# Performance work log

Measured on AMD Instinct MI355X. Metric: run time of the kernel, lower is better.

Reference implementation:

```python
import jax, jax.numpy as jnp
import numpy as np

N_HEADS = 12

def setup_inputs() -> dict:
    key = jax.random.key(0)
    k1, k2, k3 = jax.random.split(key, 3)
    B, S, W = 8, 1024, 768
    x = jax.random.normal(k1, (B, S, W), dtype=jnp.float32)
    w_qkv = jax.random.normal(k2, (W, 3 * W), dtype=jnp.float32) * (W ** -0.5)
    w_out = jax.random.normal(k3, (W, W), dtype=jnp.float32) * (W ** -0.5)
    return {"x": x, "w_qkv": w_qkv, "w_out": w_out}

def reference(x, w_qkv, w_out):
    B, S, W = x.shape
    H = N_HEADS
    D = W // H  # head_width
    scale = W ** -0.5  # NOTE: source scales by width**-0.5, not head_width**-0.5
    qkv = x @ w_qkv  # [B, S, 3W]
    q, k, v = jnp.split(qkv, 3, axis=2)
    q = q.reshape(B, S, H, D)
    k = k.reshape(B, S, H, D)
    # attn_score: [B, i, j, n]
    attn_score = jnp.einsum('binh,bjnh->bijn', q, k) * scale
    attn_weight = jax.nn.softmax(attn_score, axis=2)
    # NOTE: source uses K (not V) here — faithful reproduction of the bug.
    out = jnp.einsum('bijn,bjnh->binh', attn_weight, k)
    out = out.reshape(B, S, W)
    return out @ w_out  # dropout is identity in eval
```

## Files before the change

### kernel.cpp

```cpp
#include <hip/hip_runtime.h>

#define US unsigned short

typedef __bf16 bf16x8 __attribute__((ext_vector_type(8)));
typedef short s16x8 __attribute__((ext_vector_type(8)));
typedef short s16x4 __attribute__((ext_vector_type(4)));
typedef float f32x4 __attribute__((ext_vector_type(4)));

static __device__ __forceinline__ US f2bf(float f) {
  union { float f; unsigned u; } x; x.f = f;
  unsigned r = x.u + 0x7fffu + ((x.u >> 16) & 1u);
  return (US)(r >> 16);
}

static __device__ __forceinline__ unsigned cvtpk(float lo, float hi) {
  unsigned r;
  asm("v_cvt_pk_bf16_f32 %0, %1, %2" : "=v"(r) : "v"(lo), "v"(hi));
  return r;
}

static __device__ __forceinline__ void gload16(const US* g, US* l) {
  __builtin_amdgcn_global_load_lds(
      (const __attribute__((address_space(1))) void*)g,
      (__attribute__((address_space(3))) void*)l, 16, 0, 0);
}

__global__ __launch_bounds__(256) void cast_f32_bf16(
    const float* __restrict__ src, US* __restrict__ dst) {
  int i = blockIdx.x * 256 + threadIdx.x;
  const float4* s = (const float4*)src + (size_t)i * 2;
  float4 a = s[0], b = s[1];
  s16x8 w;
  w[0] = (short)f2bf(a.x); w[1] = (short)f2bf(a.y);
  w[2] = (short)f2bf(a.z); w[3] = (short)f2bf(a.w);
  w[4] = (short)f2bf(b.x); w[5] = (short)f2bf(b.y);
  w[6] = (short)f2bf(b.z); w[7] = (short)f2bf(b.w);
  *(s16x8*)(dst + (size_t)i * 8) = w;
}

__global__ __launch_bounds__(256) void transpose_cast_k(
    const float* __restrict__ src, US* __restrict__ dst, int R, int C,
    float scale, int nlim) {
  __shared__ float t[32][33];
  int n0 = blockIdx.x * 32, r0 = blockIdx.y * 32;
  int tx = threadIdx.x & 31, ty = threadIdx.x >> 5;
  for (int i = 0; i < 4; ++i) {
    int r = i * 8 + ty;
    t[r][tx] = src[(size_t)(r0 + r) * C + n0 + tx];
  }
  __syncthreads();
  for (int i = 0; i < 4; ++i) {
    int n = i * 8 + ty;
    float s = (n0 + n < nlim) ? scale : 1.0f;
    dst[(size_t)(n0 + n) * R + r0 + tx] = f2bf(t[tx][n] * s);
  }
}

__global__ __launch_bounds__(256) void kt_transpose(
    const US* __restrict__ QK, US* __restrict__ KT) {
  __shared__ US t[32][34];
  int bh = blockIdx.z, b = bh / 12, h = bh % 12;
  int s0 = blockIdx.x * 32, d0 = blockIdx.y * 32;
  int tx = threadIdx.x & 31, ty = threadIdx.x >> 5;
  const US* src = QK + ((size_t)b * 1024 + s0) * 1536 + 768 + h * 64 + d0;
  for (int i = 0; i < 4; ++i)
    t[i * 8 + ty][tx] = src[(size_t)(i * 8 + ty) * 1536 + tx];
  __syncthreads();
  US* dst = KT + ((size_t)bh * 64 + d0) * 1024 + s0;
  for (int i = 0; i < 4; ++i)
    dst[(size_t)(i * 8 + ty) * 1024 + tx] = t[tx][i * 8 + ty];
}

template<int OUT_BF16>
__global__ __launch_bounds__(256) void gemm_bt(
    const US* __restrict__ A, const US* __restrict__ Bt,
    void* __restrict__ Cv, int M, int N, int K) {
  __shared__ US As[2][128 * 32];
  __shared__ US Bs[2][128 * 32];
  const int tid = threadIdx.x;
  const int wave = tid >> 6, lane = tid & 63;
  const int lr = lane & 15, lg = lane >> 4;
  const int m0 = blockIdx.x * 128, n0 = blockIdx.y * 128;
  const int wr = (wave >> 1) * 64, wc = (wave & 1) * 64;
  const int srow = tid >> 2;
  const int sseg = (tid & 3) ^ (srow & 3);
  const US* gA = A + (size_t)(m0 + srow) * K + sseg * 8;
  const US* gB = Bt + (size_t)(n0 + srow) * K + sseg * 8;

  f32x4 acc[4][4];
  for (int i = 0; i < 4; ++i)
    for (int j = 0; j < 4; ++j) acc[i][j] = (f32x4){0.f, 0.f, 0.f, 0.f};

  const int nIt = K >> 5;
  for (int i = 0; i < 2; ++i) {
    gload16(gA + (size_t)i * 64 * K, &As[0][tid * 8 + i * 2048]);
    gload16(gB + (size_t)i * 64 * K, &Bs[0][tid * 8 + i * 2048]);
  }
  __syncthreads();

  for (int it = 0; it < nIt; ++it) {
    if (it + 1 < nIt) {
      int k0 = (it + 1) * 32, bb = (it + 1) & 1;
      for (int i = 0; i < 2; ++i) {
        gload16(gA + (size_t)i * 64 * K + k0, &As[bb][tid * 8 + i * 2048]);
        gload16(gB + (size_t)i * 64 * K + k0, &Bs[bb][tid * 8 + i * 2048]);
      }
    }
    const US* Ab = As[it & 1];
    const US* Bb = Bs[it & 1];
    bf16x8 af[4], bfr[4];
    for (int mi = 0; mi < 4; ++mi)
      af[mi] = *(const bf16x8*)(Ab + (wr + mi * 16 + lr) * 32 + ((lg ^ (lr & 3)) * 8));
    for (int ni = 0; ni < 4; ++ni)
      bfr[ni] = *(const bf16x8*)(Bb + (wc + ni * 16 + lr) * 32 + ((lg ^ (lr & 3)) * 8));
    for (int mi = 0; mi < 4; ++mi)
      for (int ni = 0; ni < 4; ++ni)
        acc[mi][ni] = __builtin_amdgcn_mfma_f32_16x16x32_bf16(
            af[mi], bfr[ni], acc[mi][ni], 0, 0, 0);
    __syncthreads();
  }

  for (int mi = 0; mi < 4; ++mi)
    for (int ni = 0; ni < 4; ++ni)
      for (int r = 0; r < 4; ++r) {
        size_t row = (size_t)m0 + wr + mi * 16 + lg * 4 + r;
        size_t col = (size_t)n0 + wc + ni * 16 + lr;
        float v = acc[mi][ni][r];
        if (OUT_BF16) ((US*)Cv)[row * N + col] = f2bf(v);
        else          ((float*)Cv)[row * N + col] = v;
      }
}

static __device__ __forceinline__ void softmax_route(
    const f32x4 sv[4], float& lsum, bool odd, bool hi, int laneQ0, int laneQ1,
    bf16x8& pa0v, bf16x8& pa1v) {
  float p[4][4];
#pragma unroll
  for (int ns = 0; ns < 4; ++ns)
#pragma unroll
    for (int r = 0; r < 4; ++r) {
      p[ns][r] = __builtin_amdgcn_exp2f(sv[ns][r]);
      lsum += p[ns][r];
    }
  unsigned pk00 = cvtpk(p[0][0], p[0][1]), pk01 = cvtpk(p[0][2], p[0][3]);
  unsigned pk10 = cvtpk(p[1][0], p[1][1]), pk11 = cvtpk(p[1][2], p[1][3]);
  unsigned pk20 = cvtpk(p[2][0], p[2][1]), pk21 = cvtpk(p[2][2], p[2][3]);
  unsigned pk30 = cvtpk(p[3][0], p[3][1]), pk31 = cvtpk(p[3][2], p[3][3]);
  int a0 = (int)(odd ? pk10 : pk00), a1 = (int)(odd ? pk11 : pk01);
  int a2 = (int)(odd ? pk30 : pk20), a3 = (int)(odd ? pk31 : pk21);
  int b0 = (int)(odd ? pk00 : pk10), b1 = (int)(odd ? pk01 : pk11);
  int b2 = (int)(odd ? pk20 : pk30), b3 = (int)(odd ? pk21 : pk31);
  int r0 = __shfl(a0, laneQ0), r1 = __shfl(a1, laneQ0);
  int r2 = __shfl(a2, laneQ0), r3 = __shfl(a3, laneQ0);
  int r4 = __shfl(b0, laneQ1), r5 = __shfl(b1, laneQ1);
  int r6 = __shfl(b2, laneQ1), r7 = __shfl(b3, laneQ1);
  union { unsigned u[4]; bf16x8 v; } pa0, pa1;
  pa0.u[0] = hi ? (unsigned)r4 : (unsigned)r0;
  pa0.u[1] = hi ? (unsigned)r5 : (unsigned)r1;
  pa0.u[2] = hi ? (unsigned)r0 : (unsigned)r4;
  pa0.u[3] = hi ? (unsigned)r1 : (unsigned)r5;
  pa1.u[0] = hi ? (unsigned)r6 : (unsigned)r2;
  pa1.u[1] = hi ? (unsigned)r7 : (unsigned)r3;
  pa1.u[2] = hi ? (unsigned)r2 : (unsigned)r6;
  pa1.u[3] = hi ? (unsigned)r3 : (unsigned)r7;
  pa0v = pa0.v;
  pa1v = pa1.v;
}

__global__ __launch_bounds__(256, 3) void attn_kernel(
    const US* __restrict__ QK, const US* __restrict__ KTg, US* __restrict__ AO) {
  __shared__ US Kr[2][64 * 64];
  __shared__ US Kt[2][64 * 64];
  const int tid = threadIdx.x, wave = tid >> 6, lane = tid & 63;
  const int lr = lane & 15, lg = lane >> 4;
  const int id = blockIdx.y * 8 + blockIdx.x;
  const int bh = (id & 7) * 12 + ((id >> 3) % 12);
  const int qt = id / 96;
  const int b = bh / 12, h = bh % 12;
  const int qw = qt * 128 + wave * 32;
  const size_t rowbase = (size_t)b * 1024;
  const US* Qp = QK + rowbase * 1536 + h * 64;
  const US* Kp = QK + rowbase * 1536 + 768 + h * 64;
  const US* KTp = KTg + (size_t)bh * 64 * 1024;

  const int srow = tid >> 3;
  const int sseg = (tid & 7) ^ (srow & 7);
  const US* gK = Kp + (size_t)srow * 1536 + sseg * 8;
  const US* gT = KTp + (size_t)srow * 1024 + sseg * 8;

  bf16x8 qf0[2], qf1[2];
#pragma unroll
  for (int kk = 0; kk < 2; ++kk) {
    qf0[kk] = *(const bf16x8*)(Qp + (size_t)(qw + lr) * 1536 + kk * 32 + lg * 8);
    qf1[kk] = *(const bf16x8*)(Qp + (size_t)(qw + 16 + lr) * 1536 + kk * 32 + lg * 8);
  }

  const bool odd = (lg & 1) != 0;
  const bool hi = (lg >> 1) != 0;
  const int laneQ0 = lr + 32 * (lg & 1) + 16 * (lg >> 1);
  const int laneQ1 = lr + 32 * (lg & 1) + 16 * (1 - (lg >> 1));

  float lsum0 = 0.f, lsum1 = 0.f;
  f32x4 acc0[4], acc1[4];
#pragma unroll
  for (int d = 0; d < 4; ++d) {
    acc0[d] = (f32x4){0.f, 0.f, 0.f, 0.f};
    acc1[d] = (f32x4){0.f, 0.f, 0.f, 0.f};
  }

  for (int i = 0; i < 2; ++i) {
    gload16(gK + (size_t)(i * 32) * 1536, &Kr[0][tid * 8 + i * 2048]);
    gload16(gT + (size_t)(i * 32) * 1024, &Kt[0][tid * 8 + i * 2048]);
  }
  __syncthreads();

  for (int t = 0; t < 16; ++t) {
    if (t + 1 < 16) {
      int kv0 = (t + 1) * 64, bb = (t + 1) & 1;
      for (int i = 0; i < 2; ++i) {
        gload16(gK + (size_t)(kv0 + i * 32) * 1536, &Kr[bb][tid * 8 + i * 2048]);
        gload16(gT + (size_t)(i * 32) * 1024 + kv0, &Kt[bb][tid * 8 + i * 2048]);
      }
    }
    const US* Krb = Kr[t & 1];
    const US* Ktb = Kt[t & 1];

    f32x4 sv0[4], sv1[4];
    __builtin_amdgcn_s_setprio(1);
#pragma unroll
    for (int ns = 0; ns < 4; ++ns) {
      f32x4 a0 = {0.f, 0.f, 0.f, 0.f}, a1 = {0.f, 0.f, 0.f, 0.f};
#pragma unroll
      for (int kk = 0; kk < 2; ++kk) {
        bf16x8 kf = *(const bf16x8*)(
            Krb + (ns * 16 + lr) * 64 + (((kk * 4 + lg) ^ (lr & 7)) * 8));
        a0 = __builtin_amdgcn_mfma_f32_16x16x32_bf16(kf, qf0[kk], a0, 0, 0, 0);
        a1 = __builtin_amdgcn_mfma_f32_16x16x32_bf16(kf, qf1[kk], a1, 0, 0, 0);
      }
      sv0[ns] = a0; sv1[ns] = a1;
    }
    __builtin_amdgcn_s_setprio(0);

    bf16x8 pa00, pa01, pa10, pa11;
    softmax_route(sv0, lsum0, odd, hi, laneQ0, laneQ1, pa00, pa01);
    softmax_route(sv1, lsum1, odd, hi, laneQ0, laneQ1, pa10, pa11);

    __builtin_amdgcn_s_setprio(1);
#pragma unroll
    for (int d = 0; d < 4; ++d) {
      int drow = d * 16 + lr;
      bf16x8 kf0 = *(const bf16x8*)(Ktb + drow * 64 + ((lg ^ (lr & 7)) * 8));
      bf16x8 kf1 = *(const bf16x8*)(Ktb + drow * 64 + (((4 + lg) ^ (lr & 7)) * 8));
      acc0[d] = __builtin_amdgcn_mfma_f32_16x16x32_bf16(pa00, kf0, acc0[d], 0, 0, 0);
      acc0[d] = __builtin_amdgcn_mfma_f32_16x16x32_bf16(pa01, kf1, acc0[d], 0, 0, 0);
      acc1[d] = __builtin_amdgcn_mfma_f32_16x16x32_bf16(pa10, kf0, acc1[d], 0, 0, 0);
      acc1[d] = __builtin_amdgcn_mfma_f32_16x16x32_bf16(pa11, kf1, acc1[d], 0, 0, 0);
    }
    __builtin_amdgcn_s_setprio(0);
    __syncthreads();
  }

  lsum0 += __shfl_xor(lsum0, 16);
  lsum0 += __shfl_xor(lsum0, 32);
  lsum1 += __shfl_xor(lsum1, 16);
  lsum1 += __shfl_xor(lsum1, 32);
  float inv0[4], inv1[4];
#pragma unroll
  for (int r = 0; r < 4; ++r) {
    inv0[r] = 1.0f / __shfl(lsum0, lg * 4 + r);
    inv1[r] = 1.0f / __shfl(lsum1, lg * 4 + r);
  }
#pragma unroll
  for (int d = 0; d < 4; ++d)
#pragma unroll
    for (int r = 0; r < 4; ++r) {
      size_t row0 = rowbase + qw + lg * 4 + r;
      AO[row0 * 768 + h * 64 + d * 16 + lr] = f2bf(acc0[d][r] * inv0[r]);
      size_t row1 = rowbase + qw + 16 + lg * 4 + r;
      AO[row1 * 768 + h * 64 + d * 16 + lr] = f2bf(acc1[d][r] * inv1[r]);
    }
}

extern "C" void kernel_launch(void* const* d_in, const int* in_sizes, int n_in,
                              void* d_out, int out_size, void* d_ws, size_t ws_size,
                              hipStream_t stream) {
  const float* x    = (const float*)d_in[0];
  const float* wqkv = (const float*)d_in[1];
  const float* wout = (const float*)d_in[2];
  float* out = (float*)d_out;

  US* wqkT  = (US*)d_ws;
  US* woutT = wqkT + (size_t)1536 * 768;
  US* QK    = woutT + (size_t)768 * 768;
  US* AO    = QK + (size_t)8192 * 1536;
  US* xb    = AO + (size_t)8192 * 768;
  US* KT    = xb;

  const float cexp = 0.03608439182435161f * 1.4426950408889634f;

  cast_f32_bf16<<<3072, 256, 0, stream>>>(x, xb);
  transpose_cast_k<<<dim3(48, 24), 256, 0, stream>>>(wqkv, wqkT, 768, 2304, cexp, 768);
  transpose_cast_k<<<dim3(24, 24), 256, 0, stream>>>(wout, woutT, 768, 768, 1.0f, 0);
  gemm_bt<1><<<dim3(64, 12), 256, 0, stream>>>(xb, wqkT, QK, 8192, 1536, 768);
  kt_transpose<<<dim3(32, 2, 96), 256, 0, stream>>>(QK, KT);
  attn_kernel<<<dim3(8, 96), 256, 0, stream>>>(QK, KT, AO);
  gemm_bt<0><<<dim3(64, 6), 256, 0, stream>>>(AO, woutT, out, 8192, 768, 768);
}
```

Before: 106.3 us.

## Triple-buffer LDS loads in GEMM and attention with partial vmcnt waits

Both the GEMM and the attention kernel move from double to triple LDS buffering, prefetching two tiles ahead. Each __syncthreads is replaced by an explicit s_waitcnt vmcnt(4) plus s_barrier, so the newest prefetch stays in flight across the barrier. The aim is to hide global-to-LDS latency better. In exchange, LDS use per block grows by half, which may cut occupancy (the attention kernel asks for 3 blocks per CU), and the explicit waitcnt values depend on exactly four outstanding loads per stage.

```diff
diff --git a/kernel.cpp b/kernel.cpp
--- a/kernel.cpp
+++ b/kernel.cpp
@@ -75,8 +75,8 @@
 __global__ __launch_bounds__(256) void gemm_bt(
     const US* __restrict__ A, const US* __restrict__ Bt,
     void* __restrict__ Cv, int M, int N, int K) {
-  __shared__ US As[2][128 * 32];
-  __shared__ US Bs[2][128 * 32];
+  __shared__ US As[3][4096];
+  __shared__ US Bs[3][4096];
   const int tid = threadIdx.x;
   const int wave = tid >> 6, lane = tid & 63;
   const int lr = lane & 15, lg = lane >> 4;
@@ -96,18 +96,25 @@
     gload16(gA + (size_t)i * 64 * K, &As[0][tid * 8 + i * 2048]);
     gload16(gB + (size_t)i * 64 * K, &Bs[0][tid * 8 + i * 2048]);
   }
-  __syncthreads();
-
+  for (int i = 0; i < 2; ++i) {
+    gload16(gA + (size_t)i * 64 * K + 32, &As[1][tid * 8 + i * 2048]);
+    gload16(gB + (size_t)i * 64 * K + 32, &Bs[1][tid * 8 + i * 2048]);
+  }
+  asm volatile("s_waitcnt vmcnt(4)" ::: "memory");
+  __builtin_amdgcn_s_barrier();
+  __builtin_amdgcn_sched_barrier(0);
+
+  int cur = 0, pre = 2;
   for (int it = 0; it < nIt; ++it) {
-    if (it + 1 < nIt) {
-      int k0 = (it + 1) * 32, bb = (it + 1) & 1;
+    if (it + 2 < nIt) {
+      int k0 = (it + 2) * 32;
       for (int i = 0; i < 2; ++i) {
-        gload16(gA + (size_t)i * 64 * K + k0, &As[bb][tid * 8 + i * 2048]);
-        gload16(gB + (size_t)i * 64 * K + k0, &Bs[bb][tid * 8 + i * 2048]);
+        gload16(gA + (size_t)i * 64 * K + k0, &As[pre][tid * 8 + i * 2048]);
+        gload16(gB + (size_t)i * 64 * K + k0, &Bs[pre][tid * 8 + i * 2048]);
       }
     }
-    const US* Ab = As[it & 1];
-    const US* Bb = Bs[it & 1];
+    const US* Ab = As[cur];
+    const US* Bb = Bs[cur];
     bf16x8 af[4], bfr[4];
     for (int mi = 0; mi < 4; ++mi)
       af[mi] = *(const bf16x8*)(Ab + (wr + mi * 16 + lr) * 32 + ((lg ^ (lr & 3)) * 8));
@@ -117,7 +124,12 @@
       for (int ni = 0; ni < 4; ++ni)
         acc[mi][ni] = __builtin_amdgcn_mfma_f32_16x16x32_bf16(
             af[mi], bfr[ni], acc[mi][ni], 0, 0, 0);
-    __syncthreads();
+    if (it + 2 < nIt) asm volatile("s_waitcnt vmcnt(4)" ::: "memory");
+    else              asm volatile("s_waitcnt vmcnt(0)" ::: "memory");
+    __builtin_amdgcn_s_barrier();
+    __builtin_amdgcn_sched_barrier(0);
+    cur = (cur + 1 == 3) ? 0 : cur + 1;
+    pre = (pre + 1 == 3) ? 0 : pre + 1;
   }
 
   for (int mi = 0; mi < 4; ++mi)
@@ -169,8 +181,8 @@
 
 __global__ __launch_bounds__(256, 3) void attn_kernel(
     const US* __restrict__ QK, const US* __restrict__ KTg, US* __restrict__ AO) {
-  __shared__ US Kr[2][64 * 64];
-  __shared__ US Kt[2][64 * 64];
+  __shared__ US Kr[3][4096];
+  __shared__ US Kt[3][4096];
   const int tid = threadIdx.x, wave = tid >> 6, lane = tid & 63;
   const int lr = lane & 15, lg = lane >> 4;
   const int id = blockIdx.y * 8 + blockIdx.x;
@@ -212,18 +224,25 @@
     gload16(gK + (size_t)(i * 32) * 1536, &Kr[0][tid * 8 + i * 2048]);
     gload16(gT + (size_t)(i * 32) * 1024, &Kt[0][tid * 8 + i * 2048]);
   }
-  __syncthreads();
-
+  for (int i = 0; i < 2; ++i) {
+    gload16(gK + (size_t)(64 + i * 32) * 1536, &Kr[1][tid * 8 + i * 2048]);
+    gload16(gT + (size_t)(i * 32) * 1024 + 64, &Kt[1][tid * 8 + i * 2048]);
+  }
+  asm volatile("s_waitcnt vmcnt(4)" ::: "memory");
+  __builtin_amdgcn_s_barrier();
+  __builtin_amdgcn_sched_barrier(0);
+
+  int cur = 0, pre = 2;
   for (int t = 0; t < 16; ++t) {
-    if (t + 1 < 16) {
-      int kv0 = (t + 1) * 64, bb = (t + 1) & 1;
+    if (t + 2 < 16) {
+      int kv0 = (t + 2) * 64;
       for (int i = 0; i < 2; ++i) {
-        gload16(gK + (size_t)(kv0 + i * 32) * 1536, &Kr[bb][tid * 8 + i * 2048]);
-        gload16(gT + (size_t)(i * 32) * 1024 + kv0, &Kt[bb][tid * 8 + i * 2048]);
+        gload16(gK + (size_t)(kv0 + i * 32) * 1536, &Kr[pre][tid * 8 + i * 2048]);
+        gload16(gT + (size_t)(i * 32) * 1024 + kv0, &Kt[pre][tid * 8 + i * 2048]);
       }
     }
-    const US* Krb = Kr[t & 1];
-    const US* Ktb = Kt[t & 1];
+    const US* Krb = Kr[cur];
+    const US* Ktb = Kt[cur];
 
     f32x4 sv0[4], sv1[4];
     __builtin_amdgcn_s_setprio(1);
@@ -257,7 +276,13 @@
       acc1[d] = __builtin_amdgcn_mfma_f32_16x16x32_bf16(pa11, kf1, acc1[d], 0, 0, 0);
     }
     __builtin_amdgcn_s_setprio(0);
-    __syncthreads();
+
+    if (t + 2 < 16) asm volatile("s_waitcnt vmcnt(4)" ::: "memory");
+    else            asm volatile("s_waitcnt vmcnt(0)" ::: "memory");
+    __builtin_amdgcn_s_barrier();
+    __builtin_amdgcn_sched_barrier(0);
+    cur = (cur + 1 == 3) ? 0 : cur + 1;
+    pre = (pre + 1 == 3) ? 0 : pre + 1;
   }
 
   lsum0 += __shfl_xor(lsum0, 16);
```

Result: no change. 107.7 us (+1.4%).
